# Optimization experiments

Hardware: AMD Instinct MI355X
Metric: run time of the kernel (lower is better)

Reference implementation:

```python
import jax, jax.numpy as jnp
import numpy as np

# Dimensions (all layers are mLSTM due to the constructor bug: `if w` tests the
# whole truthy `which` list, so signature=(2,1) still yields 3 mLSTM layers).
L, S, B, I = 3, 512, 4, 512      # layers, seq_len, batch, inp_dim
H, D = 8, 64                     # head_num, head_dim
HD = H * D                       # hidden dim = 512
P = 2 * I                        # up_l projection dim (m-branch p_factor = 2)
K = 4                            # causal conv kernel size
EPS = 1e-5
PNAMES = ['ln_g', 'ln_b', 'upl_w', 'upl_b', 'upr_w', 'upr_b', 'conv_w', 'conv_b',
          'wq_w', 'wq_b', 'wk_w', 'wk_b', 'wv_w', 'wv_b', 'wo_w', 'wo_b',
          'wi_w', 'wi_b', 'wf_w', 'wf_b', 'skip_w', 'gn_g', 'gn_b', 'down_w', 'down_b']


def setup_inputs() -> dict:
    key = jax.random.key(0)
    ks = iter(jax.random.split(key, 16))
    def w(shape, fan_in):
        return jax.random.normal(next(ks), shape, jnp.float32) / np.float32(np.sqrt(fan_in))
    return {
        'seq': jax.random.normal(next(ks), (S, B, I), jnp.float32),
        'ln_g': jnp.ones((L, I), jnp.float32), 'ln_b': jnp.zeros((L, I), jnp.float32),
        'upl_w': w((L, P, I), I), 'upl_b': jnp.zeros((L, P), jnp.float32),
        'upr_w': w((L, HD, I), I), 'upr_b': jnp.zeros((L, HD), jnp.float32),
        'conv_w': w((L, K), K), 'conv_b': jnp.zeros((L,), jnp.float32),
        'wq_w': w((L, HD, P), P), 'wq_b': jnp.zeros((L, HD), jnp.float32),
        'wk_w': w((L, HD, P), P), 'wk_b': jnp.zeros((L, HD), jnp.float32),
        'wv_w': w((L, HD, P), P), 'wv_b': jnp.zeros((L, HD), jnp.float32),
        'wo_w': w((L, HD, P), P), 'wo_b': jnp.zeros((L, HD), jnp.float32),
        'wi_w': w((L, H, P), P), 'wi_b': jnp.zeros((L, H), jnp.float32),
        'wf_w': w((L, H, P), P), 'wf_b': jnp.zeros((L, H), jnp.float32),
        'skip_w': w((L, HD, P), P),
        'gn_g': jnp.ones((L, HD), jnp.float32), 'gn_b': jnp.zeros((L, HD), jnp.float32),
        'down_w': w((L, I, HD), HD), 'down_b': jnp.zeros((L, I), jnp.float32),
    }


def _layernorm(x, g, b):
    mu = x.mean(-1, keepdims=True)
    v = ((x - mu) ** 2).mean(-1, keepdims=True)
    return (x - mu) / jnp.sqrt(v + EPS) * g + b


def _groupnorm(x, g, b):
    # GroupNorm(head_num, HD) on (B, HD): normalize each head's D channels
    xh = x.reshape(-1, H, D)
    mu = xh.mean(-1, keepdims=True)
    v = ((xh - mu) ** 2).mean(-1, keepdims=True)
    xn = (xh - mu) / jnp.sqrt(v + EPS)
    return (xn * g.reshape(H, D) + b.reshape(H, D)).reshape(-1, HD)


def _causal_conv(x, w, b):
    # 1-channel causal conv over the feature axis of the per-step vector (B, P)
    xp = jnp.pad(x, ((0, 0), (K - 1, 0)))
    y = b
    for k in range(K):  # K=4, static unroll
        y = y + w[k] * xp[:, k:k + x.shape[1]]
    return y


def _mlstm_step(p, x, state):
    c_, n_, m_ = state
    x_n = _layernorm(x, p['ln_g'], p['ln_b'])
    x_t = x_n @ p['upl_w'].T + p['upl_b']                 # (B, P)
    r_t = x_n @ p['upr_w'].T + p['upr_b']                 # (B, HD)
    x_c = jax.nn.silu(_causal_conv(x_t, p['conv_w'], p['conv_b']))
    q = (x_c @ p['wq_w'].T + p['wq_b']).reshape(-1, H, D)
    k = (x_c @ p['wk_w'].T + p['wk_b']).reshape(-1, H, D) / np.float32(np.sqrt(D))
    v = (x_t @ p['wv_w'].T + p['wv_b']).reshape(-1, H, D)
    i = x_c @ p['wi_w'].T + p['wi_b']                     # (B, H)
    f = x_c @ p['wf_w'].T + p['wf_b']                     # (B, H)
    o = jax.nn.sigmoid(x_t @ p['wo_w'].T + p['wo_b'])     # (B, HD)
    m = jnp.maximum(f + m_, i)                            # stabilizer
    ig = jnp.exp(i - m)
    fg = jnp.exp(f - m + m_)
    c = fg[..., None, None] * c_ + ig[..., None, None] * jnp.einsum('bhd,bhe->bhde', v, k)
    n = fg[..., None] * n_ + ig[..., None] * k
    num = jnp.einsum('bhde,bhe->bhd', c, q)
    den = jnp.maximum(jnp.abs(jnp.einsum('bhd,bhd->bh', n, q)), 1.0)[..., None]
    h = o * (num / den).reshape(-1, HD)
    out = _groupnorm(h, p['gn_g'], p['gn_b']) + x_c @ p['skip_w'].T
    out = out * jax.nn.silu(r_t)
    out = out @ p['down_w'].T + p['down_b']
    return out + x, (c, n, m)


def _forward(seq, params):
    b = seq.shape[1]
    def step(states, x_t):
        new_states = []
        inp = x_t
        for l in range(L):
            pl = {k: v[l] for k, v in params.items()}
            inp, st = _mlstm_step(pl, inp, states[l])
            new_states.append(st)
        return tuple(new_states), inp
    init = tuple((jnp.zeros((b, H, D, D), seq.dtype),
                  jnp.ones((b, H, D), seq.dtype),
                  jnp.zeros((b, H), seq.dtype)) for _ in range(L))
    _, out = jax.lax.scan(step, init, seq)
    return out  # (S, B, I)


def reference(seq, ln_g, ln_b, upl_w, upl_b, upr_w, upr_b, conv_w, conv_b,
              wq_w, wq_b, wk_w, wk_b, wv_w, wv_b, wo_w, wo_b,
              wi_w, wi_b, wf_w, wf_b, skip_w, gn_g, gn_b, down_w, down_b):
    params = dict(zip(PNAMES, [ln_g, ln_b, upl_w, upl_b, upr_w, upr_b, conv_w, conv_b,
                               wq_w, wq_b, wk_w, wk_b, wv_w, wv_b, wo_w, wo_b,
                               wi_w, wi_b, wf_w, wf_b, skip_w, gn_g, gn_b, down_w, down_b]))
    return _forward(seq, params)
```

## Files before the change

### kernel.cpp

```cpp
#include <hip/hip_runtime.h>
#include <hip/hip_bf16.h>
#include <cstdint>
#include <cstddef>

typedef short short8 __attribute__((ext_vector_type(8)));
typedef short short4v __attribute__((ext_vector_type(4)));
typedef float f32x4 __attribute__((ext_vector_type(4)));
typedef __hip_bfloat16 bf16;

#define NROW 2048
#define N1 1536
#define N2 1664
#define N3 1024
#define EPSV 1e-5f

static __device__ __forceinline__ bf16 f2bf(float v){ return __float2bfloat16(v); }
static __device__ __forceinline__ float bfbits2f(short s){
  unsigned u = ((unsigned)(unsigned short)s) << 16;
  float f; __builtin_memcpy(&f, &u, 4); return f;
}
static __device__ __forceinline__ void split_bf(float v, bf16& h, bf16& l){
  h = __float2bfloat16(v);
  l = __float2bfloat16(v - __bfloat162float(h));
}

static __device__ __forceinline__ void gload16(const bf16* g, bf16* l){
  __builtin_amdgcn_global_load_lds(
      (const __attribute__((address_space(1))) void*)(g),
      (__attribute__((address_space(3))) void*)(l), 16, 0, 0);
}

#define MFMA __builtin_amdgcn_mfma_f32_16x16x32_bf16

__global__ __launch_bounds__(256) void pack_all(
    const float* __restrict__ upl, const float* __restrict__ upr,
    const float* __restrict__ wq,  const float* __restrict__ wk,
    const float* __restrict__ skp, const float* __restrict__ wi,
    const float* __restrict__ wf,  const float* __restrict__ wv,
    const float* __restrict__ wo,  const float* __restrict__ dw,
    const float* __restrict__ uplb, const float* __restrict__ uprb,
    const float* __restrict__ wqb,  const float* __restrict__ wkb,
    const float* __restrict__ wib,  const float* __restrict__ wfb,
    const float* __restrict__ wvb,  const float* __restrict__ wob,
    const float* __restrict__ dwb,
    bf16* __restrict__ W1h, bf16* __restrict__ W1l,
    bf16* __restrict__ W2h, bf16* __restrict__ W2l,
    bf16* __restrict__ W3h, bf16* __restrict__ W3l,
    bf16* __restrict__ W4h, bf16* __restrict__ W4l,
    float* __restrict__ b1, float* __restrict__ b2,
    float* __restrict__ b3, float* __restrict__ b4)
{
  int l = blockIdx.y;
  int bx = blockIdx.x;
  if (bx < 768){
    int r = bx*2 + (threadIdx.x >> 7);
    int c4 = threadIdx.x & 127;
    const float* src = (r < 1024) ? upl + ((size_t)l*1024 + r)*512
                                  : upr + ((size_t)l*512 + (r-1024))*512;
    size_t o = ((size_t)l*N1 + r)*512 + c4*4;
    f32x4 v = *(const f32x4*)(src + c4*4);
    short4v hh, ll;
    for (int e=0;e<4;e++){ bf16 h_,l_; split_bf(v[e],h_,l_);
      hh[e] = *(short*)&h_; ll[e] = *(short*)&l_; }
    *(short4v*)(W1h+o) = hh; *(short4v*)(W1l+o) = ll;
  } else if (bx < 2432){
    int r = bx - 768;
    int c4 = threadIdx.x;
    const float* src; float sc = 1.f;
    if (r < 512)        src = wq  + ((size_t)l*512 + r)*1024;
    else if (r < 1024){ src = wk  + ((size_t)l*512 + r-512)*1024; sc = 0.125f; }
    else if (r < 1536)  src = skp + ((size_t)l*512 + r-1024)*1024;
    else if (r < 1544)  src = wi  + ((size_t)l*8   + r-1536)*1024;
    else if (r < 1552)  src = wf  + ((size_t)l*8   + r-1544)*1024;
    else src = nullptr;
    size_t o = ((size_t)l*N2 + r)*1024 + c4*4;
    f32x4 v = src ? *(const f32x4*)(src + c4*4) : (f32x4){0.f,0.f,0.f,0.f};
    short4v hh, ll;
    for (int e=0;e<4;e++){ bf16 h_,l_; split_bf(v[e]*sc,h_,l_);
      hh[e] = *(short*)&h_; ll[e] = *(short*)&l_; }
    *(short4v*)(W2h+o) = hh; *(short4v*)(W2l+o) = ll;
  } else if (bx < 3456){
    int r = bx - 2432;
    int c4 = threadIdx.x;
    const float* src = (r < 512) ? wv + ((size_t)l*512 + r)*1024
                                 : wo + ((size_t)l*512 + (r-512))*1024;
    size_t o = ((size_t)l*N3 + r)*1024 + c4*4;
    f32x4 v = *(const f32x4*)(src + c4*4);
    short4v hh, ll;
    for (int e=0;e<4;e++){ bf16 h_,l_; split_bf(v[e],h_,l_);
      hh[e] = *(short*)&h_; ll[e] = *(short*)&l_; }
    *(short4v*)(W3h+o) = hh; *(short4v*)(W3l+o) = ll;
  } else if (bx < 3712){
    int r = (bx - 3456)*2 + (threadIdx.x >> 7);
    int c4 = threadIdx.x & 127;
    const float* src = dw + ((size_t)l*512 + r)*512;
    size_t o = ((size_t)l*512 + r)*512 + c4*4;
    f32x4 v = *(const f32x4*)(src + c4*4);
    short4v hh, ll;
    for (int e=0;e<4;e++){ bf16 h_,l_; split_bf(v[e],h_,l_);
      hh[e] = *(short*)&h_; ll[e] = *(short*)&l_; }
    *(short4v*)(W4h+o) = hh; *(short4v*)(W4l+o) = ll;
  } else {
    for (int j = threadIdx.x; j < N1; j += 256)
      b1[l*N1+j] = (j < 1024) ? uplb[l*1024+j] : uprb[l*512+j-1024];
    for (int j = threadIdx.x; j < N2; j += 256){
      float v = 0.f;
      if (j < 512)        v = wqb[l*512+j];
      else if (j < 1024)  v = wkb[l*512+j-512]*0.125f;
      else if (j < 1536)  v = 0.f;
      else if (j < 1544)  v = wib[l*8+j-1536];
      else if (j < 1552)  v = wfb[l*8+j-1544];
      b2[l*N2+j] = v;
    }
    for (int j = threadIdx.x; j < N3; j += 256)
      b3[l*N3+j] = (j < 512) ? wvb[l*512+j] : wob[l*512+j-512];
    for (int j = threadIdx.x; j < 512; j += 256)
      b4[l*512+j] = dwb[l*512+j];
  }
}

static __device__ __forceinline__ void gemm_core(
    bf16* __restrict__ sm,
    int bx, int by,
    const bf16* __restrict__ Ah, const bf16* __restrict__ Al,
    const bf16* __restrict__ Wh, const bf16* __restrict__ Wl,
    const float* __restrict__ bias, float* __restrict__ Cf,
    bf16* __restrict__ Cbh, bf16* __restrict__ Cbl,
    const float* __restrict__ resid, int N, int K, int lda)
{
  int tid = threadIdx.x;
  int lane = tid & 63, w = tid >> 6;
  int wr = w >> 2, wc = w & 3;
  int m0 = by*128, n0 = bx*128;
  int srow = tid >> 2, sslot = tid & 3;
  int gcol = ((sslot ^ (srow & 3)) * 8);
  const bf16* gAh = Ah + (size_t)(m0 + srow)*lda + gcol;
  const bf16* gAl = Al + (size_t)(m0 + srow)*lda + gcol;
  const bf16* gBh = Wh + (size_t)(n0 + srow)*K + gcol;
  const bf16* gBl = Wl + (size_t)(n0 + srow)*K + gcol;

  f32x4 acc[4][2];
  for (int i=0;i<4;i++) for (int j=0;j<2;j++) acc[i][j] = (f32x4){0.f,0.f,0.f,0.f};

  int r = lane & 15, g = lane >> 4;
  int xs = (g ^ (r & 3)) * 8;
  int aoff[4], boff[2];
  for (int mi=0;mi<4;mi++) aoff[mi] = (wr*64 + mi*16 + r)*32 + xs;
  for (int ni=0;ni<2;ni++) boff[ni] = (wc*32 + ni*16 + r)*32 + xs;

  int nt = K >> 5;
#define STAGE_T(base, kk) do{ bf16* _d = sm + (base) + tid*8; \
    gload16(gAh + (kk), _d); \
    gload16(gAl + (kk), _d + 4096); \
    gload16(gBh + (kk), _d + 8192); \
    gload16(gBl + (kk), _d + 12288); }while(0)

  STAGE_T(0, 0);
  asm volatile("s_waitcnt vmcnt(0)" ::: "memory");
  __builtin_amdgcn_s_barrier();

  for (int t = 0; t < nt; ++t){
    int cb = (t & 1) * 16384;
    if (t + 1 < nt) STAGE_T(16384 - cb, (t+1)*32);
    const bf16* sA = sm + cb;
    short8 ah[4], al[4], bh2[2], bl2[2];
    for (int mi=0;mi<4;mi++){
      ah[mi] = *(const short8*)(sA + aoff[mi]);
      al[mi] = *(const short8*)(sA + 4096 + aoff[mi]);
    }
    for (int ni=0;ni<2;ni++){
      bh2[ni] = *(const short8*)(sA + 8192 + boff[ni]);
      bl2[ni] = *(const short8*)(sA + 12288 + boff[ni]);
    }
    for (int mi=0;mi<4;mi++) for (int ni=0;ni<2;ni++)
      acc[mi][ni] = MFMA(ah[mi], bh2[ni], acc[mi][ni],0,0,0);
    for (int mi=0;mi<4;mi++) for (int ni=0;ni<2;ni++)
      acc[mi][ni] = MFMA(al[mi], bh2[ni], acc[mi][ni],0,0,0);
    for (int mi=0;mi<4;mi++) for (int ni=0;ni<2;ni++)
      acc[mi][ni] = MFMA(ah[mi], bl2[ni], acc[mi][ni],0,0,0);
    asm volatile("s_waitcnt vmcnt(0)" ::: "memory");
    __builtin_amdgcn_s_barrier();
  }
#undef STAGE_T

  for (int mi=0;mi<4;mi++) for (int ni=0;ni<2;ni++){
    int col = n0 + wc*32 + ni*16 + r;
    float bv = bias ? bias[col] : 0.f;
    for (int j=0;j<4;j++){
      int row = m0 + wr*64 + mi*16 + g*4 + j;
      float v = acc[mi][ni][j] + bv;
      size_t o = (size_t)row*N + col;
      if (resid) v += resid[o];
      if (Cf) Cf[o] = v;
      if (Cbh) split_bf(v, Cbh[o], Cbl[o]);
    }
  }
}

static __device__ __forceinline__ void gemm_core64(
    bf16* __restrict__ sm,
    int bx, int by,
    const bf16* __restrict__ Ah, const bf16* __restrict__ Al,
    const bf16* __restrict__ Wh, const bf16* __restrict__ Wl,
    const float* __restrict__ bias, float* __restrict__ Cf,
    bf16* __restrict__ Cbh, bf16* __restrict__ Cbl,
    const float* __restrict__ resid, int N, int K, int lda)
{
  int tid = threadIdx.x;
  int lane = tid & 63, w = tid >> 6;
  int m0 = by*64, n0 = bx*128;
  int srow = tid >> 2, sslot = tid & 3;
  int gcol = ((sslot ^ (srow & 3)) * 8);
  const bf16* gAh = Ah + (size_t)(m0 + srow)*lda + gcol;
  const bf16* gAl = Al + (size_t)(m0 + srow)*lda + gcol;
  const bf16* gBh = Wh + (size_t)(n0 + srow)*K + gcol;
  const bf16* gBl = Wl + (size_t)(n0 + srow)*K + gcol;
  size_t pstr = (size_t)64*K;

  f32x4 acc[4][2];
  for (int i=0;i<4;i++) for (int j=0;j<2;j++) acc[i][j] = (f32x4){0.f,0.f,0.f,0.f};

  int r = lane & 15, g = lane >> 4;
  int xs = (g ^ (r & 3)) * 8;
  int aoff[4], boff[2];
  for (int mi=0;mi<4;mi++) aoff[mi] = (mi*16 + r)*32 + xs;
  for (int ni=0;ni<2;ni++) boff[ni] = (w*32 + ni*16 + r)*32 + xs;

  int nt = K >> 5;
#define STAGE64(base, kk) do{ bf16* _d = sm + (base) + tid*8; \
    gload16(gAh + (kk), _d); \
    gload16(gAl + (kk), _d + 2048); \
    gload16(gBh + (kk), _d + 4096);  gload16(gBh + (kk) + pstr, _d + 6144); \
    gload16(gBl + (kk), _d + 8192);  gload16(gBl + (kk) + pstr, _d + 10240); }while(0)

  STAGE64(0, 0);
  asm volatile("s_waitcnt vmcnt(0)" ::: "memory");
  __builtin_amdgcn_s_barrier();

  for (int t = 0; t < nt; ++t){
    int cb = (t & 1) * 12288;
    if (t + 1 < nt) STAGE64(12288 - cb, (t+1)*32);
    const bf16* sA = sm + cb;
    short8 ah[4], al[4], bh2[2], bl2[2];
    for (int mi=0;mi<4;mi++){
      ah[mi] = *(const short8*)(sA + aoff[mi]);
      al[mi] = *(const short8*)(sA + 2048 + aoff[mi]);
    }
    for (int ni=0;ni<2;ni++){
      bh2[ni] = *(const short8*)(sA + 4096 + boff[ni]);
      bl2[ni] = *(const short8*)(sA + 8192 + boff[ni]);
    }
    for (int mi=0;mi<4;mi++) for (int ni=0;ni<2;ni++)
      acc[mi][ni] = MFMA(ah[mi], bh2[ni], acc[mi][ni],0,0,0);
    for (int mi=0;mi<4;mi++) for (int ni=0;ni<2;ni++)
      acc[mi][ni] = MFMA(al[mi], bh2[ni], acc[mi][ni],0,0,0);
    for (int mi=0;mi<4;mi++) for (int ni=0;ni<2;ni++)
      acc[mi][ni] = MFMA(ah[mi], bl2[ni], acc[mi][ni],0,0,0);
    asm volatile("s_waitcnt vmcnt(0)" ::: "memory");
    __builtin_amdgcn_s_barrier();
  }
#undef STAGE64

  for (int mi=0;mi<4;mi++) for (int ni=0;ni<2;ni++){
    int col = n0 + w*32 + ni*16 + r;
    float bv = bias ? bias[col] : 0.f;
    for (int j=0;j<4;j++){
      int row = m0 + mi*16 + g*4 + j;
      float v = acc[mi][ni][j] + bv;
      size_t o = (size_t)row*N + col;
      if (resid) v += resid[o];
      if (Cf) Cf[o] = v;
      if (Cbh) split_bf(v, Cbh[o], Cbl[o]);
    }
  }
}

__global__ __launch_bounds__(256) void gemm_s64(
    const bf16* __restrict__ Ah, const bf16* __restrict__ Al,
    const bf16* __restrict__ Wh, const bf16* __restrict__ Wl,
    const float* __restrict__ bias, float* __restrict__ Cf,
    bf16* __restrict__ Cbh, bf16* __restrict__ Cbl,
    const float* __restrict__ resid, int N, int K, int lda, int nbx)
{
  __shared__ bf16 sm[2*12288];
  int id = blockIdx.x;
  int cpx = gridDim.x >> 3;
  int swz = (id & 7)*cpx + (id >> 3);
  int by = swz / nbx, bx = swz - by*nbx;
  gemm_core64(sm, bx, by, Ah, Al, Wh, Wl, bias, Cf, Cbh, Cbl, resid, N, K, lda);
}

__global__ __launch_bounds__(512) void gemm23(
    const bf16* __restrict__ A2h, const bf16* __restrict__ A2l,
    const bf16* __restrict__ W2h, const bf16* __restrict__ W2l,
    const float* __restrict__ b2,
    bf16* __restrict__ c2h, bf16* __restrict__ c2l,
    const bf16* __restrict__ A3h, const bf16* __restrict__ A3l,
    const bf16* __restrict__ W3h, const bf16* __restrict__ W3l,
    const float* __restrict__ b3,
    bf16* __restrict__ c3h, bf16* __restrict__ c3l)
{
  __shared__ bf16 sm[2*4*4096];
  int id = blockIdx.x;
  int cpx = gridDim.x >> 3;
  int swz = (id & 7)*cpx + (id >> 3);
  int by = swz / 21, bx = swz - by*21;
  if (bx < 13)
    gemm_core(sm, bx, by, A2h, A2l, W2h, W2l, b2, nullptr, c2h, c2l,
              nullptr, N2, 1024, 1024);
  else
    gemm_core(sm, bx-13, by, A3h, A3l, W3h, W3l, b3, nullptr, c3h, c3l,
              nullptr, N3, 1024, N1);
}

__global__ __launch_bounds__(256) void ln_kernel(const float* __restrict__ x,
    const float* __restrict__ g, const float* __restrict__ bt,
    bf16* __restrict__ xnh, bf16* __restrict__ xnl)
{
  int row = blockIdx.x, t = threadIdx.x;
  float v0 = x[(size_t)row*512 + t], v1 = x[(size_t)row*512 + 256 + t];
  float s = v0 + v1, ss = v0*v0 + v1*v1;
  for (int m=1; m<64; m<<=1){ s += __shfl_xor(s,m); ss += __shfl_xor(ss,m); }
  __shared__ float sh[8];
  int w = t >> 6, lane = t & 63;
  if (lane == 0){ sh[w] = s; sh[4+w] = ss; }
  __syncthreads();
  s = sh[0]+sh[1]+sh[2]+sh[3]; ss = sh[4]+sh[5]+sh[6]+sh[7];
  float mu = s*(1.f/512.f), var = ss*(1.f/512.f) - mu*mu;
  float rs = rsqrtf(var + EPSV);
  float y0 = (v0-mu)*rs*g[t]     + bt[t];
  float y1 = (v1-mu)*rs*g[256+t] + bt[256+t];
  split_bf(y0, xnh[(size_t)row*512 + t],       xnl[(size_t)row*512 + t]);
  split_bf(y1, xnh[(size_t)row*512 + 256 + t], xnl[(size_t)row*512 + 256 + t]);
}

__global__ __launch_bounds__(256) void conv_kernel(
    const bf16* __restrict__ c1h, const bf16* __restrict__ c1l,
    const float* __restrict__ cw, const float* __restrict__ cb,
    bf16* __restrict__ xch, bf16* __restrict__ xcl)
{
  int row = blockIdx.x;
  size_t rb = (size_t)row*N1;
  float w0=cw[0], w1=cw[1], w2=cw[2], w3=cw[3], bb=cb[0];
  int j0 = threadIdx.x*4;
  float x[7];
  for (int k=0;k<3;k++){
    int j = j0-3+k;
    x[k] = (j>=0) ? (bfbits2f(*(const short*)(c1h+rb+j)) +
                     bfbits2f(*(const short*)(c1l+rb+j))) : 0.f;
  }
  short4v h4 = *(const short4v*)(c1h+rb+j0);
  short4v l4 = *(const short4v*)(c1l+rb+j0);
  for (int k=0;k<4;k++) x[3+k] = bfbits2f(h4[k]) + bfbits2f(l4[k]);
  for (int i=0;i<4;i++){
    float y = bb + w0*x[i] + w1*x[i+1] + w2*x[i+2] + w3*x[i+3];
    float sg = 1.f/(1.f + __expf(-y));
    size_t o = (size_t)row*1024 + j0 + i;
    split_bf(y*sg, xch[o], xcl[o]);
  }
}

__global__ __launch_bounds__(512) void prep_kernel(
    const bf16* __restrict__ c3h, const bf16* __restrict__ c3l,
    const bf16* __restrict__ c2h, const bf16* __restrict__ c2l,
    bf16* __restrict__ vTh, bf16* __restrict__ vTl,
    float* __restrict__ rowt, float* __restrict__ colt)
{
  int bh = blockIdx.y, b = bh >> 3, h = bh & 7;
  if (blockIdx.x < 8){
    __shared__ short th[64*66], tl[64*66];
    int s0 = blockIdx.x*64;
    int sl = threadIdx.x >> 3, d8 = (threadIdx.x & 7)*8;
    size_t i = (size_t)((s0+sl)*4+b)*N3 + h*64 + d8;
    short8 hv = *(const short8*)(c3h+i);
    short8 lv = *(const short8*)(c3l+i);
    for (int e=0;e<8;e++){
      th[sl*66 + d8+e] = hv[e];
      tl[sl*66 + d8+e] = lv[e];
    }
    __syncthreads();
    int dl = threadIdx.x >> 3, s8 = (threadIdx.x & 7)*8;
    short8 oh, ol;
    for (int e=0;e<8;e++){
      oh[e] = th[(s8+e)*66 + dl];
      ol[e] = tl[(s8+e)*66 + dl];
    }
    size_t o = ((size_t)bh*64 + dl)*512 + s0 + s8;
    *(short8*)(vTh+o) = oh;
    *(short8*)(vTl+o) = ol;
    return;
  }
  if (threadIdx.x >= 64) return;
  int lane = threadIdx.x;
  double fv[8]; float iv[8];
  for (int j=0;j<8;j++){
    int t = lane*8 + j;
    size_t ro = (size_t)(t*4+b)*N2;
    fv[j] = (double)(bfbits2f(*(const short*)(c2h+ro+1544+h)) +
                     bfbits2f(*(const short*)(c2l+ro+1544+h)));
    iv[j] = bfbits2f(*(const short*)(c2h+ro+1536+h)) +
            bfbits2f(*(const short*)(c2l+ro+1536+h));
  }
  double ps[8]; double s = 0.0;
  for (int j=0;j<8;j++){ s += fv[j]; ps[j] = s; }
  double run = s;
  for (int o=1;o<64;o<<=1){
    double u = __shfl_up(run, o);
    if (lane >= o) run += u;
  }
  double excl = run - s;
  float ct[8];
  for (int j=0;j<8;j++){
    ct[j] = (float)((double)iv[j] - (excl + ps[j]));
    colt[bh*512 + lane*8 + j] = ct[j];
  }
  float pm[8]; float mm = -3.0e38f;
  for (int j=0;j<8;j++){ mm = fmaxf(mm, ct[j]); pm[j] = mm; }
  float incl = mm;
  for (int o=1;o<64;o<<=1){
    float u = __shfl_up(incl, o);
    if (lane >= o) incl = fmaxf(incl, u);
  }
  float ex = __shfl_up(incl, 1);
  if (lane == 0) ex = -3.0e38f;
  for (int j=0;j<8;j++){
    float inc = fmaxf(ex, pm[j]);
    rowt[bh*512 + lane*8 + j] = -fmaxf(0.f, inc);
  }
}

__global__ __launch_bounds__(256) void attn_kernel(
    const bf16* __restrict__ c2h, const bf16* __restrict__ c2l,
    const bf16* __restrict__ vTh, const bf16* __restrict__ vTl,
    const float* __restrict__ rowt, const float* __restrict__ colt,
    float* __restrict__ num, float* __restrict__ denp)
{
  __shared__ bf16 Ph[32*64], Pl[32*64];
  __shared__ float cts[512];
  int lane = threadIdx.x & 63, w = threadIdx.x >> 6;
  int x = blockIdx.x;
  int tb = (x & 1) ? (15 - (x >> 1)) : (x >> 1);
  int bh = blockIdx.y, b = bh >> 3, h = bh & 7;
  int t0 = tb*32;

  cts[threadIdx.x]       = colt[bh*512 + threadIdx.x];
  cts[256 + threadIdx.x] = colt[bh*512 + 256 + threadIdx.x];
  __syncthreads();

  int r = lane & 15, g = lane >> 4;
  int rq = g*4;

  short8 qh[2][2], ql[2][2];
  for (int mi=0;mi<2;mi++) for (int k0=0;k0<2;k0++){
    size_t off = (size_t)((t0+mi*16+r)*4+b)*N2 + h*64 + k0*32 + g*8;
    qh[mi][k0] = *(const short8*)(c2h+off);
    ql[mi][k0] = *(const short8*)(c2l+off);
  }
  float rtv[2][4];
  for (int mi=0;mi<2;mi++) for (int j=0;j<4;j++)
    rtv[mi][j] = rowt[bh*512 + t0 + mi*16 + rq + j];

  f32x4 accPV[2];
  for (int i=0;i<2;i++) accPV[i] = (f32x4){0.f,0.f,0.f,0.f};
  float rsum[2][4];
  for (int i=0;i<2;i++) for (int j=0;j<4;j++) rsum[i][j] = 0.f;

  int nsb = (tb >> 1) + 1;
  for (int sb=0; sb<nsb; ++sb){
    int s0 = sb*64;
    f32x4 acc[2];
    for (int i=0;i<2;i++) acc[i] = (f32x4){0.f,0.f,0.f,0.f};
    short8 kh[2], kl[2];
    for (int k0=0;k0<2;k0++){
      size_t off = (size_t)((s0+w*16+r)*4+b)*N2 + 512 + h*64 + k0*32 + g*8;
      kh[k0] = *(const short8*)(c2h+off);
      kl[k0] = *(const short8*)(c2l+off);
    }
    for (int k0=0;k0<2;k0++){
      for (int mi=0;mi<2;mi++) acc[mi] = MFMA(qh[mi][k0], kh[k0], acc[mi],0,0,0);
      for (int mi=0;mi<2;mi++) acc[mi] = MFMA(ql[mi][k0], kh[k0], acc[mi],0,0,0);
      for (int mi=0;mi<2;mi++) acc[mi] = MFMA(qh[mi][k0], kl[k0], acc[mi],0,0,0);
    }
    int sl = w*16 + r;
    int s = s0 + sl;
    float ctv = cts[s];
    for (int mi=0;mi<2;mi++){
      for (int j=0;j<4;j++){
        int tloc = mi*16 + rq + j;
        int t = t0 + tloc;
        float wg = (s <= t) ? __expf(rtv[mi][j] + ctv) : 0.f;
        float gv = acc[mi][j] * wg;
        rsum[mi][j] += gv;
        int col = ((((sl>>3) ^ (tloc&7))<<3) | (sl&7));
        split_bf(gv, Ph[tloc*64+col], Pl[tloc*64+col]);
      }
    }
    __syncthreads();
    short8 vh[2], vl[2];
    for (int k0=0;k0<2;k0++){
      size_t off = ((size_t)bh*64 + w*16 + r)*512 + s0 + k0*32 + g*8;
      vh[k0] = *(const short8*)(vTh+off);
      vl[k0] = *(const short8*)(vTl+off);
    }
    for (int k0=0;k0<2;k0++){
      short8 ph[2], pl[2];
      for (int mi=0;mi<2;mi++){
        int tloc = mi*16 + r;
        int slot = (k0*4 + g) ^ (tloc&7);
        ph[mi] = *(const short8*)(&Ph[tloc*64 + slot*8]);
        pl[mi] = *(const short8*)(&Pl[tloc*64 + slot*8]);
      }
      for (int mi=0;mi<2;mi++) accPV[mi] = MFMA(ph[mi], vh[k0], accPV[mi],0,0,0);
      for (int mi=0;mi<2;mi++) accPV[mi] = MFMA(pl[mi], vh[k0], accPV[mi],0,0,0);
      for (int mi=0;mi<2;mi++) accPV[mi] = MFMA(ph[mi], vl[k0], accPV[mi],0,0,0);
    }
    __syncthreads();
  }

  for (int mi=0;mi<2;mi++)
    for (int j=0;j<4;j++){
      int t = t0 + mi*16 + rq + j;
      num[((size_t)bh*512 + t)*64 + w*16 + r] = accPV[mi][j];
    }
  for (int mi=0;mi<2;mi++)
    for (int j=0;j<4;j++){
      float v = rsum[mi][j];
      v += __shfl_xor(v,1); v += __shfl_xor(v,2);
      v += __shfl_xor(v,4); v += __shfl_xor(v,8);
      if (r == 0){
        int t = t0 + mi*16 + rq + j;
        denp[((size_t)bh*512 + t)*4 + w] = v;
      }
    }
}

__global__ __launch_bounds__(512) void h_kernel(
    const float* __restrict__ num, const float* __restrict__ denp,
    const float* __restrict__ rowt,
    const bf16* __restrict__ c2h, const bf16* __restrict__ c2l,
    const bf16* __restrict__ c3h, const bf16* __restrict__ c3l,
    const bf16* __restrict__ c1h, const bf16* __restrict__ c1l,
    const float* __restrict__ gng, const float* __restrict__ gnb,
    bf16* __restrict__ oph, bf16* __restrict__ opl)
{
  int row = blockIdx.x, t = row >> 2, b = row & 3;
  int h = threadIdx.x >> 6, d = threadIdx.x & 63;
  int bh = b*8 + h;
  size_t bt = (size_t)bh*512 + t;
  size_t qo = (size_t)row*N2 + h*64 + d;
  float qs = bfbits2f(*(const short*)(c2h+qo)) + bfbits2f(*(const short*)(c2l+qo));
  for (int m=1; m<64; m<<=1) qs += __shfl_xor(qs, m);
  float dn = __expf(rowt[bt]) * qs;
  for (int p=0; p<4; p++) dn += denp[bt*4 + p];
  dn = fmaxf(fabsf(dn), 1.f);
  float nv = num[bt*64 + d];
  size_t io = (size_t)row*N3 + 512 + h*64 + d;
  float ov = bfbits2f(*(const short*)(c3h+io)) + bfbits2f(*(const short*)(c3l+io));
  float o = 1.f/(1.f + __expf(-ov));
  float hv = o * nv / dn;
  float s = hv, ss = hv*hv;
  for (int m=1; m<64; m<<=1){ s += __shfl_xor(s,m); ss += __shfl_xor(ss,m); }
  float mu = s*(1.f/64.f), var = ss*(1.f/64.f) - mu*mu;
  float gn = (hv - mu)*rsqrtf(var + EPSV)*gng[h*64+d] + gnb[h*64+d];
  size_t ks = (size_t)row*N2 + 1024 + h*64 + d;
  float sk = bfbits2f(*(const short*)(c2h+ks)) + bfbits2f(*(const short*)(c2l+ks));
  size_t kr = (size_t)row*N1 + 1024 + h*64 + d;
  float rv = bfbits2f(*(const short*)(c1h+kr)) + bfbits2f(*(const short*)(c1l+kr));
  float y = (gn + sk) * (rv/(1.f + __expf(-rv)));
  size_t oo = (size_t)row*512 + h*64 + d;
  split_bf(y, oph[oo], opl[oo]);
}

extern "C" void kernel_launch(void* const* d_in, const int* in_sizes, int n_in,
                              void* d_out, int out_size, void* d_ws, size_t ws_size,
                              hipStream_t stream)
{
  (void)in_sizes; (void)n_in; (void)out_size; (void)ws_size;
  const float* seq    = (const float*)d_in[0];
  const float* ln_g   = (const float*)d_in[1];
  const float* ln_b   = (const float*)d_in[2];
  const float* upl_w  = (const float*)d_in[3];
  const float* upl_b  = (const float*)d_in[4];
  const float* upr_w  = (const float*)d_in[5];
  const float* upr_b  = (const float*)d_in[6];
  const float* conv_w = (const float*)d_in[7];
  const float* conv_b = (const float*)d_in[8];
  const float* wq_w   = (const float*)d_in[9];
  const float* wq_b   = (const float*)d_in[10];
  const float* wk_w   = (const float*)d_in[11];
  const float* wk_b   = (const float*)d_in[12];
  const float* wv_w   = (const float*)d_in[13];
  const float* wv_b   = (const float*)d_in[14];
  const float* wo_w   = (const float*)d_in[15];
  const float* wo_b   = (const float*)d_in[16];
  const float* wi_w   = (const float*)d_in[17];
  const float* wi_b   = (const float*)d_in[18];
  const float* wf_w   = (const float*)d_in[19];
  const float* wf_b   = (const float*)d_in[20];
  const float* skip_w = (const float*)d_in[21];
  const float* gn_g   = (const float*)d_in[22];
  const float* gn_b   = (const float*)d_in[23];
  const float* down_w = (const float*)d_in[24];
  const float* down_b = (const float*)d_in[25];

  char* ws = (char*)d_ws;
  size_t off = 0;
  auto alloc = [&](size_t bytes)->char*{
    char* p = ws + off; off = (off + bytes + 255) & ~(size_t)255; return p;
  };
  bf16*  W1h = (bf16*)alloc((size_t)3*N1*512*2);
  bf16*  W1l = (bf16*)alloc((size_t)3*N1*512*2);
  bf16*  W2h = (bf16*)alloc((size_t)3*N2*1024*2);
  bf16*  W2l = (bf16*)alloc((size_t)3*N2*1024*2);
  bf16*  W3h = (bf16*)alloc((size_t)3*N3*1024*2);
  bf16*  W3l = (bf16*)alloc((size_t)3*N3*1024*2);
  bf16*  W4h = (bf16*)alloc((size_t)3*512*512*2);
  bf16*  W4l = (bf16*)alloc((size_t)3*512*512*2);
  float* b1  = (float*)alloc((size_t)3*N1*4);
  float* b2  = (float*)alloc((size_t)3*N2*4);
  float* b3  = (float*)alloc((size_t)3*N3*4);
  float* b4  = (float*)alloc((size_t)3*512*4);
  bf16*  xnh = (bf16*)alloc((size_t)NROW*512*2);
  bf16*  xnl = (bf16*)alloc((size_t)NROW*512*2);
  bf16*  c1h = (bf16*)alloc((size_t)NROW*N1*2);
  bf16*  c1l = (bf16*)alloc((size_t)NROW*N1*2);
  bf16*  xch = (bf16*)alloc((size_t)NROW*1024*2);
  bf16*  xcl = (bf16*)alloc((size_t)NROW*1024*2);
  bf16*  c2h = (bf16*)alloc((size_t)NROW*N2*2);
  bf16*  c2l = (bf16*)alloc((size_t)NROW*N2*2);
  bf16*  c3h = (bf16*)alloc((size_t)NROW*N3*2);
  bf16*  c3l = (bf16*)alloc((size_t)NROW*N3*2);
  bf16*  vTh = (bf16*)alloc((size_t)32*64*512*2);
  bf16*  vTl = (bf16*)alloc((size_t)32*64*512*2);
  float* rowt= (float*)alloc((size_t)32*512*4);
  float* colt= (float*)alloc((size_t)32*512*4);
  float* denp= (float*)alloc((size_t)32*512*4*4);
  float* num = (float*)alloc((size_t)32*512*64*4);
  bf16*  oph = (bf16*)alloc((size_t)NROW*512*2);
  bf16*  opl = (bf16*)alloc((size_t)NROW*512*2);
  float* xA  = (float*)alloc((size_t)NROW*512*4);
  float* xB  = (float*)alloc((size_t)NROW*512*4);

  pack_all<<<dim3(3713,3), 256, 0, stream>>>(
      upl_w, upr_w, wq_w, wk_w, skip_w, wi_w, wf_w, wv_w, wo_w, down_w,
      upl_b, upr_b, wq_b, wk_b, wi_b, wf_b, wv_b, wo_b, down_b,
      W1h, W1l, W2h, W2l, W3h, W3l, W4h, W4l, b1, b2, b3, b4);

  for (int l = 0; l < 3; l++){
    const float* x_in = (l == 0) ? seq : ((l == 1) ? xA : xB);
    float* x_out = (l == 0) ? xA : ((l == 1) ? xB : (float*)d_out);

    ln_kernel<<<NROW, 256, 0, stream>>>(x_in, ln_g + l*512, ln_b + l*512, xnh, xnl);
    gemm_s64<<<32*12, 256, 0, stream>>>(
        xnh, xnl, W1h + (size_t)l*N1*512, W1l + (size_t)l*N1*512,
        b1 + l*N1, nullptr, c1h, c1l, nullptr, N1, 512, 512, 12);
    conv_kernel<<<NROW, 256, 0, stream>>>(c1h, c1l, conv_w + l*4, conv_b + l,
                                          xch, xcl);
    gemm23<<<21*16, 512, 0, stream>>>(
        xch, xcl, W2h + (size_t)l*N2*1024, W2l + (size_t)l*N2*1024, b2 + l*N2,
        c2h, c2l,
        c1h, c1l, W3h + (size_t)l*N3*1024, W3l + (size_t)l*N3*1024, b3 + l*N3,
        c3h, c3l);
    prep_kernel<<<dim3(9,32), 512, 0, stream>>>(c3h, c3l, c2h, c2l,
                                                vTh, vTl, rowt, colt);
    attn_kernel<<<dim3(16,32), 256, 0, stream>>>(c2h, c2l, vTh, vTl,
                                                 rowt, colt, num, denp);
    h_kernel<<<NROW, 512, 0, stream>>>(num, denp, rowt, c2h, c2l, c3h, c3l,
                                       c1h, c1l, gn_g + l*512, gn_b + l*512,
                                       oph, opl);
    gemm_s64<<<32*4, 256, 0, stream>>>(
        oph, opl, W4h + (size_t)l*512*512, W4l + (size_t)l*512*512,
        b4 + l*512, x_out, nullptr, nullptr, x_in, 512, 512, 512, 4);
  }
}
```

Before: 387.7 us.

## Fuse h_kernel epilogue into attn_kernel via shared-memory num/den

Moves the normalization, output gating, GroupNorm, skip and SiLU epilogue into the attention kernel. Numerator and denominator partials now stay in shared memory instead of going to global buffers, and the q-sum is taken from the q fragments already loaded. This removes one launch per layer and the global round trip of num/denp. In exchange the attention kernel uses more LDS and does more work at its tail, and its per-thread epilogue reads are vectorized to short8.

```diff
diff --git a/kernel.cpp b/kernel.cpp
--- a/kernel.cpp
+++ b/kernel.cpp
@@ -433,10 +433,16 @@
     const bf16* __restrict__ c2h, const bf16* __restrict__ c2l,
     const bf16* __restrict__ vTh, const bf16* __restrict__ vTl,
     const float* __restrict__ rowt, const float* __restrict__ colt,
-    float* __restrict__ num, float* __restrict__ denp)
+    const bf16* __restrict__ c3h, const bf16* __restrict__ c3l,
+    const bf16* __restrict__ c1h, const bf16* __restrict__ c1l,
+    const float* __restrict__ gng, const float* __restrict__ gnb,
+    bf16* __restrict__ oph, bf16* __restrict__ opl)
 {
   __shared__ bf16 Ph[32*64], Pl[32*64];
   __shared__ float cts[512];
+  __shared__ float numS[32][64];
+  __shared__ float denS[32][4];
+  __shared__ float qsS[32];
   int lane = threadIdx.x & 63, w = threadIdx.x >> 6;
   int x = blockIdx.x;
   int tb = (x & 1) ? (15 - (x >> 1)) : (x >> 1);
@@ -445,7 +451,6 @@
 
   cts[threadIdx.x]       = colt[bh*512 + threadIdx.x];
   cts[256 + threadIdx.x] = colt[bh*512 + 256 + threadIdx.x];
-  __syncthreads();
 
   int r = lane & 15, g = lane >> 4;
   int rq = g*4;
@@ -456,9 +461,19 @@
     qh[mi][k0] = *(const short8*)(c2h+off);
     ql[mi][k0] = *(const short8*)(c2l+off);
   }
+  for (int mi=0;mi<2;mi++){
+    float qp = 0.f;
+    for (int k0=0;k0<2;k0++)
+      for (int e=0;e<8;e++)
+        qp += bfbits2f(qh[mi][k0][e]) + bfbits2f(ql[mi][k0][e]);
+    qp += __shfl_xor(qp, 16);
+    qp += __shfl_xor(qp, 32);
+    if (w == 0 && g == 0) qsS[mi*16 + r] = qp;
+  }
   float rtv[2][4];
   for (int mi=0;mi<2;mi++) for (int j=0;j<4;j++)
     rtv[mi][j] = rowt[bh*512 + t0 + mi*16 + rq + j];
+  __syncthreads();
 
   f32x4 accPV[2];
   for (int i=0;i<2;i++) accPV[i] = (f32x4){0.f,0.f,0.f,0.f};
@@ -518,57 +533,55 @@
   }
 
   for (int mi=0;mi<2;mi++)
-    for (int j=0;j<4;j++){
-      int t = t0 + mi*16 + rq + j;
-      num[((size_t)bh*512 + t)*64 + w*16 + r] = accPV[mi][j];
-    }
+    for (int j=0;j<4;j++)
+      numS[mi*16 + rq + j][w*16 + r] = accPV[mi][j];
   for (int mi=0;mi<2;mi++)
     for (int j=0;j<4;j++){
       float v = rsum[mi][j];
       v += __shfl_xor(v,1); v += __shfl_xor(v,2);
       v += __shfl_xor(v,4); v += __shfl_xor(v,8);
-      if (r == 0){
-        int t = t0 + mi*16 + rq + j;
-        denp[((size_t)bh*512 + t)*4 + w] = v;
-      }
-    }
-}
-
-__global__ __launch_bounds__(512) void h_kernel(
-    const float* __restrict__ num, const float* __restrict__ denp,
-    const float* __restrict__ rowt,
-    const bf16* __restrict__ c2h, const bf16* __restrict__ c2l,
-    const bf16* __restrict__ c3h, const bf16* __restrict__ c3l,
-    const bf16* __restrict__ c1h, const bf16* __restrict__ c1l,
-    const float* __restrict__ gng, const float* __restrict__ gnb,
-    bf16* __restrict__ oph, bf16* __restrict__ opl)
-{
-  int row = blockIdx.x, t = row >> 2, b = row & 3;
-  int h = threadIdx.x >> 6, d = threadIdx.x & 63;
-  int bh = b*8 + h;
-  size_t bt = (size_t)bh*512 + t;
-  size_t qo = (size_t)row*N2 + h*64 + d;
-  float qs = bfbits2f(*(const short*)(c2h+qo)) + bfbits2f(*(const short*)(c2l+qo));
-  for (int m=1; m<64; m<<=1) qs += __shfl_xor(qs, m);
-  float dn = __expf(rowt[bt]) * qs;
-  for (int p=0; p<4; p++) dn += denp[bt*4 + p];
+      if (r == 0) denS[mi*16 + rq + j][w] = v;
+    }
+  __syncthreads();
+
+  int tl = (w << 3) | (lane >> 3);
+  int d8 = (lane & 7) * 8;
+  int t = t0 + tl;
+  int row = t*4 + b;
+  float dn = __expf(rowt[bh*512 + t]) * qsS[tl]
+           + denS[tl][0] + denS[tl][1] + denS[tl][2] + denS[tl][3];
   dn = fmaxf(fabsf(dn), 1.f);
-  float nv = num[bt*64 + d];
-  size_t io = (size_t)row*N3 + 512 + h*64 + d;
-  float ov = bfbits2f(*(const short*)(c3h+io)) + bfbits2f(*(const short*)(c3l+io));
-  float o = 1.f/(1.f + __expf(-ov));
-  float hv = o * nv / dn;
-  float s = hv, ss = hv*hv;
-  for (int m=1; m<64; m<<=1){ s += __shfl_xor(s,m); ss += __shfl_xor(ss,m); }
-  float mu = s*(1.f/64.f), var = ss*(1.f/64.f) - mu*mu;
-  float gn = (hv - mu)*rsqrtf(var + EPSV)*gng[h*64+d] + gnb[h*64+d];
-  size_t ks = (size_t)row*N2 + 1024 + h*64 + d;
-  float sk = bfbits2f(*(const short*)(c2h+ks)) + bfbits2f(*(const short*)(c2l+ks));
-  size_t kr = (size_t)row*N1 + 1024 + h*64 + d;
-  float rv = bfbits2f(*(const short*)(c1h+kr)) + bfbits2f(*(const short*)(c1l+kr));
-  float y = (gn + sk) * (rv/(1.f + __expf(-rv)));
-  size_t oo = (size_t)row*512 + h*64 + d;
-  split_bf(y, oph[oo], opl[oo]);
+  short8 ovh = *(const short8*)(c3h + (size_t)row*N3 + 512 + h*64 + d8);
+  short8 ovl = *(const short8*)(c3l + (size_t)row*N3 + 512 + h*64 + d8);
+  float hv[8], s_ = 0.f, ss = 0.f;
+  for (int e=0;e<8;e++){
+    float ov = bfbits2f(ovh[e]) + bfbits2f(ovl[e]);
+    float o = 1.f/(1.f + __expf(-ov));
+    float v = o * numS[tl][d8+e] / dn;
+    hv[e] = v; s_ += v; ss += v*v;
+  }
+  s_ += __shfl_xor(s_,1); ss += __shfl_xor(ss,1);
+  s_ += __shfl_xor(s_,2); ss += __shfl_xor(ss,2);
+  s_ += __shfl_xor(s_,4); ss += __shfl_xor(ss,4);
+  float mu = s_*(1.f/64.f), var = ss*(1.f/64.f) - mu*mu;
+  float rs = rsqrtf(var + EPSV);
+  short8 skh = *(const short8*)(c2h + (size_t)row*N2 + 1024 + h*64 + d8);
+  short8 skl = *(const short8*)(c2l + (size_t)row*N2 + 1024 + h*64 + d8);
+  short8 rvh = *(const short8*)(c1h + (size_t)row*N1 + 1024 + h*64 + d8);
+  short8 rvl = *(const short8*)(c1l + (size_t)row*N1 + 1024 + h*64 + d8);
+  short8 yh, yl;
+  for (int e=0;e<8;e++){
+    float gn = (hv[e]-mu)*rs*gng[h*64+d8+e] + gnb[h*64+d8+e];
+    float sk = bfbits2f(skh[e]) + bfbits2f(skl[e]);
+    float rv = bfbits2f(rvh[e]) + bfbits2f(rvl[e]);
+    float y = (gn + sk) * (rv/(1.f + __expf(-rv)));
+    bf16 h_, l_;
+    split_bf(y, h_, l_);
+    yh[e] = *(short*)&h_; yl[e] = *(short*)&l_;
+  }
+  size_t oo = (size_t)row*512 + h*64 + d8;
+  *(short8*)(oph+oo) = yh;
+  *(short8*)(opl+oo) = yl;
 }
 
 extern "C" void kernel_launch(void* const* d_in, const int* in_sizes, int n_in,
@@ -634,8 +647,6 @@
   bf16*  vTl = (bf16*)alloc((size_t)32*64*512*2);
   float* rowt= (float*)alloc((size_t)32*512*4);
   float* colt= (float*)alloc((size_t)32*512*4);
-  float* denp= (float*)alloc((size_t)32*512*4*4);
-  float* num = (float*)alloc((size_t)32*512*64*4);
   bf16*  oph = (bf16*)alloc((size_t)NROW*512*2);
   bf16*  opl = (bf16*)alloc((size_t)NROW*512*2);
   float* xA  = (float*)alloc((size_t)NROW*512*4);
@@ -664,10 +675,9 @@
     prep_kernel<<<dim3(9,32), 512, 0, stream>>>(c3h, c3l, c2h, c2l,
                                                 vTh, vTl, rowt, colt);
     attn_kernel<<<dim3(16,32), 256, 0, stream>>>(c2h, c2l, vTh, vTl,
-                                                 rowt, colt, num, denp);
-    h_kernel<<<NROW, 512, 0, stream>>>(num, denp, rowt, c2h, c2l, c3h, c3l,
-                                       c1h, c1l, gn_g + l*512, gn_b + l*512,
-                                       oph, opl);
+                                                 rowt, colt, c3h, c3l, c1h, c1l,
+                                                 gn_g + l*512, gn_b + l*512,
+                                                 oph, opl);
     gemm_s64<<<32*4, 256, 0, stream>>>(
         oph, opl, W4h + (size_t)l*512*512, W4l + (size_t)l*512*512,
         b4 + l*512, x_out, nullptr, nullptr, x_in, 512, 512, 512, 4);
```

Result: faster. 376.1 us (-3.0%).
